# Kernel tuning notes

Measured on AMD Instinct MI355X. Metric: run time of the kernel, lower is better.

The kernel has to match this reference:

```python
import jax, jax.numpy as jnp
import numpy as np

ALPHA = 0.5      # AverageIteration limiting_alpha = max_alpha = 0.5
MAX_ITER = 50    # solver max_iter (tol-based early stop replaced by fixed count)
M = 0.1          # monotonicity margin: mu_inf(W) = 1 - m


def _make_W(A, m):
    # NEMON inf-norm parameterization: keep off-diagonal of A, set diagonal
    # W_ii = (1-m) - sum_j |offdiag_ij| so that mu_inf(W) = 1 - m exactly.
    d = jnp.diag(A)
    off = A - jnp.diag(d)
    T = jnp.sum(jnp.abs(off), axis=1)
    return off + jnp.diag((1.0 - m) - T)


def setup_inputs() -> dict:
    key = jax.random.key(0)
    k1, k2, k3, k4 = jax.random.split(key, 4)
    B, in_dim, out_dim = 16384, 784, 100
    x = jax.random.uniform(k1, (B, in_dim), dtype=jnp.float32)          # pixel-like in [0,1]
    A = jax.random.normal(k2, (out_dim, out_dim), jnp.float32) / np.sqrt(out_dim)
    U = jax.random.normal(k3, (out_dim, in_dim), jnp.float32) / np.sqrt(in_dim)
    b = jax.random.normal(k4, (out_dim,), jnp.float32) * 0.01
    eps = jnp.float32(0.1)  # input perturbation radius
    return {"x": x, "eps": eps, "A": A, "U": U, "b": b}


def reference(x, eps, A, U, b):
    W = _make_W(A, M)
    # elementwise positive/negative parts for the mixed-monotone (interval) embedding
    Wp, Wn = jnp.maximum(W, 0.0), jnp.minimum(W, 0.0)
    Up, Un = jnp.maximum(U, 0.0), jnp.minimum(U, 0.0)

    xmax, xmin = jnp.max(x), jnp.min(x)
    xh = jnp.minimum(x + eps, xmax)   # upper interval endpoint
    xl = jnp.maximum(x - eps, xmin)   # lower interval endpoint

    # injection terms Ux + b, computed once (constant across iterations)
    u  = x  @ U.T + b                              # [B, out]
    uh = xh @ Up.T + xl @ Un.T + b                 # upper-bound injection
    ul = xl @ Up.T + xh @ Un.T + b                 # lower-bound injection

    z0 = jnp.zeros_like(u)

    def step(carry, _):
        z, zh, zl = carry
        zn  = jax.nn.relu(z  @ W.T  + u)
        zhn = jax.nn.relu(zh @ Wp.T + zl @ Wn.T + uh)
        zln = jax.nn.relu(zl @ Wp.T + zh @ Wn.T + ul)
        new = ((1.0 - ALPHA) * z  + ALPHA * zn,
               (1.0 - ALPHA) * zh + ALPHA * zhn,
               (1.0 - ALPHA) * zl + ALPHA * zln)
        return new, None

    (z, zh, zl), _ = jax.lax.scan(step, (z0, z0, z0), None, length=MAX_ITER)
    return jnp.stack([z, zh, zl])  # [3, B, out]: nominal / upper / lower fixed points
```

## Files before the change

kernel.cpp:

```cpp
#include <hip/hip_runtime.h>
#include <math.h>

#define B_ROWS 16384
#define IN_DIM 784
#define OUT_DIM 100
#define NITER 50

#define TB  256
#define RPB 32
#define WKP 112

typedef float  f32x4   __attribute__((ext_vector_type(4)));
typedef float  f32x16  __attribute__((ext_vector_type(16)));
typedef short  short8  __attribute__((ext_vector_type(8)));
typedef unsigned int uint4v __attribute__((ext_vector_type(4)));

#define MFMA32 __builtin_amdgcn_mfma_f32_32x32x16_bf16

#define ZP_OFF 0
#define SH_OFF 8192
#define SL_OFF 16384
#define DH_OFF 24576
#define DL_OFF 32768
#define BUF_SZ 40960
#define LDS_TOTAL 81920

#define WPAD_F 16
#define UPAD_F (16 + 128 * WKP)

__device__ __forceinline__ unsigned enc_f(float f) {
  unsigned u = __float_as_uint(f);
  return (u & 0x80000000u) ? ~u : (u | 0x80000000u);
}
__device__ __forceinline__ float dec_f(unsigned e) {
  unsigned u = (e & 0x80000000u) ? (e ^ 0x80000000u) : ~e;
  return __uint_as_float(u);
}
__device__ __forceinline__ unsigned pk(float f1, float f0) {
  return __builtin_amdgcn_perm(__float_as_uint(f1), __float_as_uint(f0), 0x07060302u);
}
__device__ __forceinline__ short8 pack8(f32x4 a, f32x4 b) {
  uint4v u;
  u[0] = pk(a[1], a[0]); u[1] = pk(a[3], a[2]);
  u[2] = pk(b[1], b[0]); u[3] = pk(b[3], b[2]);
  return __builtin_bit_cast(short8, u);
}

__global__ void k_init(unsigned* wsu) {
  wsu[0] = 0u;
  wsu[1] = 0xFFFFFFFFu;
}

__global__ void k_minmax(const float4* __restrict__ x4, unsigned* __restrict__ wsu) {
  float mx = -3.4e38f, mn = 3.4e38f;
  const int n4 = (B_ROWS * IN_DIM) / 4;
  for (int i = blockIdx.x * blockDim.x + threadIdx.x; i < n4; i += gridDim.x * blockDim.x) {
    float4 v = x4[i];
    mx = fmaxf(mx, fmaxf(fmaxf(v.x, v.y), fmaxf(v.z, v.w)));
    mn = fminf(mn, fminf(fminf(v.x, v.y), fminf(v.z, v.w)));
  }
  #pragma unroll
  for (int o = 32; o; o >>= 1) {
    mx = fmaxf(mx, __shfl_xor(mx, o));
    mn = fminf(mn, __shfl_xor(mn, o));
  }
  __shared__ float smx[8], smn[8];
  int wid = threadIdx.x >> 6;
  if ((threadIdx.x & 63) == 0) { smx[wid] = mx; smn[wid] = mn; }
  __syncthreads();
  if (threadIdx.x == 0) {
    int nw = blockDim.x >> 6;
    for (int w = 1; w < nw; ++w) { mx = fmaxf(mx, smx[w]); mn = fminf(mn, smn[w]); }
    atomicMax(&wsu[0], enc_f(mx));
    atomicMin(&wsu[1], enc_f(mn));
  }
}

__global__ void k_wbuild(const float* __restrict__ A, float* __restrict__ Wpad) {
  int c = threadIdx.x;
  if (c < OUT_DIM) {
    float T = 0.f;
    for (int j = 0; j < OUT_DIM; ++j)
      if (j != c) T += fabsf(A[c * OUT_DIM + j]);
    for (int k = 0; k < WKP; ++k) {
      float v = 0.f;
      if (k < OUT_DIM) v = (k == c) ? (0.9f - T) : A[c * OUT_DIM + k];
      Wpad[c * WKP + k] = v;
    }
  } else if (c < 128) {
    for (int k = 0; k < WKP; ++k) Wpad[c * WKP + k] = 0.f;
  }
}

__global__ void k_upad(const float* __restrict__ U, float* __restrict__ Upad) {
  int i = blockIdx.x * blockDim.x + threadIdx.x;
  if (i < 128 * IN_DIM) {
    int n = i / IN_DIM;
    Upad[i] = (n < OUT_DIM) ? U[i] : 0.f;
  }
}

__launch_bounds__(TB, 2)
__global__ void k_main(const float* __restrict__ x, const float* __restrict__ epsp,
                       const float* __restrict__ bvec, const float* __restrict__ Wpad,
                       const unsigned* __restrict__ wsu, const float* __restrict__ Upad,
                       float* __restrict__ out) {
  extern __shared__ char lds[];
  const int t    = threadIdx.x;
  const int l    = t & 63;
  const int nt   = t >> 6;
  const int lm   = l & 31;
  const int hi   = l >> 5;
  const int r0   = blockIdx.x * RPB;
  const int mrow = lm;
  const int nbase = nt * 32;

  short8 whc[7], wlc[7];
  #pragma unroll
  for (int c = 0; c < 7; ++c) {
    const float* wp = Wpad + (nbase + lm) * WKP + c * 16 + hi * 8;
    f32x4 a = *(const f32x4*)wp;
    f32x4 b = *(const f32x4*)(wp + 4);
    whc[c] = pack8(a, b);
    f32x4 alo, blo;
    #pragma unroll
    for (int j = 0; j < 4; ++j) {
      alo[j] = a[j] - __uint_as_float(__float_as_uint(a[j]) & 0xffff0000u);
      blo[j] = b[j] - __uint_as_float(__float_as_uint(b[j]) & 0xffff0000u);
    }
    wlc[c] = pack8(alo, blo);
  }

  for (int e = t * 16; e < BUF_SZ; e += TB * 16)
    *(f32x4*)(lds + e) = (f32x4){0.f, 0.f, 0.f, 0.f};
  __syncthreads();

  const float eps  = epsp[0];
  const float xmax = dec_f(wsu[0]);
  const float xmin = dec_f(wsu[1]);

  f32x16 inj_u, inj_s, inj_d;
  #pragma unroll
  for (int r = 0; r < 16; ++r) {
    int n = nbase + (r & 3) + 8 * (r >> 2) + 4 * hi;
    float bn = (n < OUT_DIM) ? bvec[n] : 0.f;
    inj_u[r] = bn; inj_s[r] = bn; inj_d[r] = 0.f;
  }

  for (int c = 0; c < 49; ++c) {
    const int koff = c * 16 + hi * 8;
    const float* xp = x + (size_t)(r0 + mrow) * IN_DIM + koff;
    f32x4 x0 = *(const f32x4*)xp;
    f32x4 x1 = *(const f32x4*)(xp + 4);
    f32x4 xs0, xs1, xd0, xd1;
    #pragma unroll
    for (int j = 0; j < 4; ++j) {
      float h0 = fminf(x0[j] + eps, xmax), l0 = fmaxf(x0[j] - eps, xmin);
      float h1 = fminf(x1[j] + eps, xmax), l1 = fmaxf(x1[j] - eps, xmin);
      xs0[j] = 0.5f * (h0 + l0); xd0[j] = 0.5f * (h0 - l0);
      xs1[j] = 0.5f * (h1 + l1); xd1[j] = 0.5f * (h1 - l1);
    }
    short8 xa  = pack8(x0, x1);
    short8 xsa = pack8(xs0, xs1);
    short8 xda = pack8(xd0, xd1);

    const float* up = Upad + (size_t)(nbase + lm) * IN_DIM + koff;
    f32x4 u0 = *(const f32x4*)up;
    f32x4 u1 = *(const f32x4*)(up + 4);
    short8 ub = pack8(u0, u1);
    short8 au = __builtin_bit_cast(short8,
        __builtin_bit_cast(uint4v, ub) & 0x7fff7fffu);

    inj_u = MFMA32(ub, xa,  inj_u, 0, 0, 0);
    inj_s = MFMA32(ub, xsa, inj_s, 0, 0, 0);
    inj_d = MFMA32(au, xda, inj_d, 0, 0, 0);
  }

  f32x16 zc, sc, dc;
  #pragma unroll
  for (int r = 0; r < 16; ++r) { zc[r] = 0.f; sc[r] = 0.f; dc[r] = 0.f; }

  const int kr    = ((mrow & 7) << 1) | ((mrow >> 3) & 1);
  const int sbase = mrow * 256;

  #pragma unroll 1
  for (int it = 0; it < NITER; ++it) {
    const int rbase = (it & 1) ? BUF_SZ : 0;
    const int wbase = rbase ^ BUF_SZ;
    const bool last = (it == NITER - 1);

    {
      f32x16 az = inj_u;
      #pragma unroll
      for (int c = 0; c < 7; ++c) {
        const char* rp_ = lds + rbase + sbase + (((2 * c + hi) ^ kr) << 4);
        short8 z8 = *(const short8*)(rp_ + ZP_OFF);
        az = MFMA32(whc[c], z8, az, 0, 0, 0);
      }
      #pragma unroll
      for (int r = 0; r < 16; ++r)
        zc[r] = 0.5f * zc[r] + 0.5f * fmaxf(az[r], 0.f);
    }
    if (!last) {
      #pragma unroll
      for (int qd = 0; qd < 4; ++qd) {
        const int r = qd * 4;
        char* wp_ = lds + wbase + sbase + (((nt * 4 + qd) ^ kr) << 4) + hi * 8;
        *(uint2*)(wp_ + ZP_OFF) =
            make_uint2(pk(zc[r + 1], zc[r]), pk(zc[r + 3], zc[r + 2]));
      }
    }
    {
      f32x16 as4 = inj_s, ad4 = inj_d;
      #pragma unroll
      for (int c = 0; c < 7; ++c) {
        const char* rp_ = lds + rbase + sbase + (((2 * c + hi) ^ kr) << 4);
        short8 sh8 = *(const short8*)(rp_ + SH_OFF);
        short8 sl8 = *(const short8*)(rp_ + SL_OFF);
        short8 dh8 = *(const short8*)(rp_ + DH_OFF);
        short8 dl8 = *(const short8*)(rp_ + DL_OFF);
        short8 wh = whc[c], wl = wlc[c];
        uint4v whu = __builtin_bit_cast(uint4v, wh);
        short8 awh = __builtin_bit_cast(short8, whu & 0x7fff7fffu);
        short8 awl = __builtin_bit_cast(short8,
            __builtin_bit_cast(uint4v, wl) ^ (whu & 0x80008000u));
        as4 = MFMA32(wh,  sh8, as4, 0, 0, 0);
        as4 = MFMA32(wl,  sh8, as4, 0, 0, 0);
        as4 = MFMA32(wh,  sl8, as4, 0, 0, 0);
        ad4 = MFMA32(awh, dh8, ad4, 0, 0, 0);
        ad4 = MFMA32(awl, dh8, ad4, 0, 0, 0);
        ad4 = MFMA32(awh, dl8, ad4, 0, 0, 0);
      }
      #pragma unroll
      for (int r = 0; r < 16; ++r) {
        float rp = fmaxf(as4[r] + ad4[r], 0.f);
        float rm = fmaxf(as4[r] - ad4[r], 0.f);
        sc[r] = 0.5f * sc[r] + 0.25f * (rp + rm);
        dc[r] = 0.5f * dc[r] + 0.25f * (rp - rm);
      }
    }
    if (!last) {
      #pragma unroll
      for (int qd = 0; qd < 4; ++qd) {
        const int r = qd * 4;
        char* wp_ = lds + wbase + sbase + (((nt * 4 + qd) ^ kr) << 4) + hi * 8;
        f32x4 hi4, lo4;
        #pragma unroll
        for (int j = 0; j < 4; ++j) {
          hi4[j] = __uint_as_float(__float_as_uint(sc[r + j]) & 0xffff0000u);
          lo4[j] = sc[r + j] - hi4[j];
        }
        *(uint2*)(wp_ + SH_OFF) = make_uint2(pk(hi4[1], hi4[0]), pk(hi4[3], hi4[2]));
        *(uint2*)(wp_ + SL_OFF) = make_uint2(pk(lo4[1], lo4[0]), pk(lo4[3], lo4[2]));
        #pragma unroll
        for (int j = 0; j < 4; ++j) {
          hi4[j] = __uint_as_float(__float_as_uint(dc[r + j]) & 0xffff0000u);
          lo4[j] = dc[r + j] - hi4[j];
        }
        *(uint2*)(wp_ + DH_OFF) = make_uint2(pk(hi4[1], hi4[0]), pk(hi4[3], hi4[2]));
        *(uint2*)(wp_ + DL_OFF) = make_uint2(pk(lo4[1], lo4[0]), pk(lo4[3], lo4[2]));
      }
      __syncthreads();
    }
  }

  const size_t PL = (size_t)B_ROWS * OUT_DIM;
  #pragma unroll
  for (int qd = 0; qd < 4; ++qd) {
    const int nb = nbase + qd * 8 + hi * 4;
    if (nb < OUT_DIM) {
      const int r = qd * 4;
      const size_t gi = (size_t)(r0 + mrow) * OUT_DIM + nb;
      f32x4 zv, hv, lv;
      #pragma unroll
      for (int j = 0; j < 4; ++j) {
        zv[j] = zc[r + j];
        hv[j] = sc[r + j] + dc[r + j];
        lv[j] = sc[r + j] - dc[r + j];
      }
      *(f32x4*)(out + gi)          = zv;
      *(f32x4*)(out + PL + gi)     = hv;
      *(f32x4*)(out + 2 * PL + gi) = lv;
    }
  }
}

extern "C" void kernel_launch(void* const* d_in, const int* in_sizes, int n_in,
                              void* d_out, int out_size, void* d_ws, size_t ws_size,
                              hipStream_t stream) {
  const float* x   = (const float*)d_in[0];
  const float* eps = (const float*)d_in[1];
  const float* A   = (const float*)d_in[2];
  const float* U   = (const float*)d_in[3];
  const float* b   = (const float*)d_in[4];
  float* out = (float*)d_out;

  unsigned* wsu  = (unsigned*)d_ws;
  float*    Wpad = (float*)d_ws + WPAD_F;
  float*    Upad = (float*)d_ws + UPAD_F;

  (void)hipFuncSetAttribute((const void*)k_main,
                            hipFuncAttributeMaxDynamicSharedMemorySize, LDS_TOTAL);

  k_init<<<1, 1, 0, stream>>>(wsu);
  k_minmax<<<1024, 256, 0, stream>>>((const float4*)x, wsu);
  k_wbuild<<<1, 128, 0, stream>>>(A, Wpad);
  k_upad<<<(128 * IN_DIM + 255) / 256, 256, 0, stream>>>(U, Upad);
  k_main<<<B_ROWS / RPB, TB, LDS_TOTAL, stream>>>(x, eps, b, Wpad, wsu, Upad, out);
}
```

Measured before the change: 251.6 us.

## Use two waves per block, each computing two 32-column output tiles

Halves the block to 128 threads so each wave owns 64 output columns (two 32x32 MFMA tiles) and reuses each LDS-loaded z/s/d fragment for both tiles. This halves LDS reads per MFMA and the number of waves that synchronise per iteration. In exchange it doubles per-thread register use (weights, accumulators, state), relaxes launch bounds to one block per SIMD, and halves the waves available to hide MFMA and LDS latency.

After: 305.6 us. 1.21x slower.

```diff
diff --git a/kernel.cpp b/kernel.cpp
--- a/kernel.cpp
+++ b/kernel.cpp
@@ -6,7 +6,7 @@
 #define OUT_DIM 100
 #define NITER 50
 
-#define TB  256
+#define TB  128
 #define RPB 32
 #define WKP 112
 
@@ -100,7 +100,7 @@
   }
 }
 
-__launch_bounds__(TB, 2)
+__launch_bounds__(TB, 1)
 __global__ void k_main(const float* __restrict__ x, const float* __restrict__ epsp,
                        const float* __restrict__ bvec, const float* __restrict__ Wpad,
                        const unsigned* __restrict__ wsu, const float* __restrict__ Upad,
@@ -113,22 +113,24 @@
   const int hi   = l >> 5;
   const int r0   = blockIdx.x * RPB;
   const int mrow = lm;
-  const int nbase = nt * 32;
-
-  short8 whc[7], wlc[7];
-  #pragma unroll
-  for (int c = 0; c < 7; ++c) {
-    const float* wp = Wpad + (nbase + lm) * WKP + c * 16 + hi * 8;
-    f32x4 a = *(const f32x4*)wp;
-    f32x4 b = *(const f32x4*)(wp + 4);
-    whc[c] = pack8(a, b);
-    f32x4 alo, blo;
-    #pragma unroll
-    for (int j = 0; j < 4; ++j) {
-      alo[j] = a[j] - __uint_as_float(__float_as_uint(a[j]) & 0xffff0000u);
-      blo[j] = b[j] - __uint_as_float(__float_as_uint(b[j]) & 0xffff0000u);
-    }
-    wlc[c] = pack8(alo, blo);
+
+  short8 whc[2][7], wlc[2][7];
+  #pragma unroll
+  for (int q = 0; q < 2; ++q) {
+    #pragma unroll
+    for (int c = 0; c < 7; ++c) {
+      const float* wp = Wpad + (nt * 64 + q * 32 + lm) * WKP + c * 16 + hi * 8;
+      f32x4 a = *(const f32x4*)wp;
+      f32x4 b = *(const f32x4*)(wp + 4);
+      whc[q][c] = pack8(a, b);
+      f32x4 alo, blo;
+      #pragma unroll
+      for (int j = 0; j < 4; ++j) {
+        alo[j] = a[j] - __uint_as_float(__float_as_uint(a[j]) & 0xffff0000u);
+        blo[j] = b[j] - __uint_as_float(__float_as_uint(b[j]) & 0xffff0000u);
+      }
+      wlc[q][c] = pack8(alo, blo);
+    }
   }
 
   for (int e = t * 16; e < BUF_SZ; e += TB * 16)
@@ -139,12 +141,15 @@
   const float xmax = dec_f(wsu[0]);
   const float xmin = dec_f(wsu[1]);
 
-  f32x16 inj_u, inj_s, inj_d;
-  #pragma unroll
-  for (int r = 0; r < 16; ++r) {
-    int n = nbase + (r & 3) + 8 * (r >> 2) + 4 * hi;
-    float bn = (n < OUT_DIM) ? bvec[n] : 0.f;
-    inj_u[r] = bn; inj_s[r] = bn; inj_d[r] = 0.f;
+  f32x16 inj_u[2], inj_s[2], inj_d[2];
+  #pragma unroll
+  for (int q = 0; q < 2; ++q) {
+    #pragma unroll
+    for (int r = 0; r < 16; ++r) {
+      int n = nt * 64 + q * 32 + (r & 3) + 8 * (r >> 2) + 4 * hi;
+      float bn = (n < OUT_DIM) ? bvec[n] : 0.f;
+      inj_u[q][r] = bn; inj_s[q][r] = bn; inj_d[q][r] = 0.f;
+    }
   }
 
   for (int c = 0; c < 49; ++c) {
@@ -164,21 +169,26 @@
     short8 xsa = pack8(xs0, xs1);
     short8 xda = pack8(xd0, xd1);
 
-    const float* up = Upad + (size_t)(nbase + lm) * IN_DIM + koff;
-    f32x4 u0 = *(const f32x4*)up;
-    f32x4 u1 = *(const f32x4*)(up + 4);
-    short8 ub = pack8(u0, u1);
-    short8 au = __builtin_bit_cast(short8,
-        __builtin_bit_cast(uint4v, ub) & 0x7fff7fffu);
-
-    inj_u = MFMA32(ub, xa,  inj_u, 0, 0, 0);
-    inj_s = MFMA32(ub, xsa, inj_s, 0, 0, 0);
-    inj_d = MFMA32(au, xda, inj_d, 0, 0, 0);
-  }
-
-  f32x16 zc, sc, dc;
-  #pragma unroll
-  for (int r = 0; r < 16; ++r) { zc[r] = 0.f; sc[r] = 0.f; dc[r] = 0.f; }
+    #pragma unroll
+    for (int q = 0; q < 2; ++q) {
+      const float* up = Upad + (size_t)(nt * 64 + q * 32 + lm) * IN_DIM + koff;
+      f32x4 u0 = *(const f32x4*)up;
+      f32x4 u1 = *(const f32x4*)(up + 4);
+      short8 ub = pack8(u0, u1);
+      short8 au = __builtin_bit_cast(short8,
+          __builtin_bit_cast(uint4v, ub) & 0x7fff7fffu);
+      inj_u[q] = MFMA32(ub, xa,  inj_u[q], 0, 0, 0);
+      inj_s[q] = MFMA32(ub, xsa, inj_s[q], 0, 0, 0);
+      inj_d[q] = MFMA32(au, xda, inj_d[q], 0, 0, 0);
+    }
+  }
+
+  f32x16 zc[2], sc[2], dc[2];
+  #pragma unroll
+  for (int q = 0; q < 2; ++q) {
+    #pragma unroll
+    for (int r = 0; r < 16; ++r) { zc[q][r] = 0.f; sc[q][r] = 0.f; dc[q][r] = 0.f; }
+  }
 
   const int kr    = ((mrow & 7) << 1) | ((mrow >> 3) & 1);
   const int sbase = mrow * 256;
@@ -190,28 +200,35 @@
     const bool last = (it == NITER - 1);
 
     {
-      f32x16 az = inj_u;
+      f32x16 az0 = inj_u[0], az1 = inj_u[1];
       #pragma unroll
       for (int c = 0; c < 7; ++c) {
         const char* rp_ = lds + rbase + sbase + (((2 * c + hi) ^ kr) << 4);
         short8 z8 = *(const short8*)(rp_ + ZP_OFF);
-        az = MFMA32(whc[c], z8, az, 0, 0, 0);
-      }
-      #pragma unroll
-      for (int r = 0; r < 16; ++r)
-        zc[r] = 0.5f * zc[r] + 0.5f * fmaxf(az[r], 0.f);
+        az0 = MFMA32(whc[0][c], z8, az0, 0, 0, 0);
+        az1 = MFMA32(whc[1][c], z8, az1, 0, 0, 0);
+      }
+      #pragma unroll
+      for (int r = 0; r < 16; ++r) {
+        zc[0][r] = 0.5f * zc[0][r] + 0.5f * fmaxf(az0[r], 0.f);
+        zc[1][r] = 0.5f * zc[1][r] + 0.5f * fmaxf(az1[r], 0.f);
+      }
     }
     if (!last) {
       #pragma unroll
-      for (int qd = 0; qd < 4; ++qd) {
-        const int r = qd * 4;
-        char* wp_ = lds + wbase + sbase + (((nt * 4 + qd) ^ kr) << 4) + hi * 8;
-        *(uint2*)(wp_ + ZP_OFF) =
-            make_uint2(pk(zc[r + 1], zc[r]), pk(zc[r + 3], zc[r + 2]));
+      for (int q = 0; q < 2; ++q) {
+        #pragma unroll
+        for (int qd = 0; qd < 4; ++qd) {
+          const int r = qd * 4;
+          char* wp_ = lds + wbase + sbase +
+                      ((((nt * 2 + q) * 4 + qd) ^ kr) << 4) + hi * 8;
+          *(uint2*)(wp_ + ZP_OFF) =
+              make_uint2(pk(zc[q][r + 1], zc[q][r]), pk(zc[q][r + 3], zc[q][r + 2]));
+        }
       }
     }
     {
-      f32x16 as4 = inj_s, ad4 = inj_d;
+      f32x16 as0 = inj_s[0], ad0 = inj_d[0], as1 = inj_s[1], ad1 = inj_d[1];
       #pragma unroll
       for (int c = 0; c < 7; ++c) {
         const char* rp_ = lds + rbase + sbase + (((2 * c + hi) ^ kr) << 4);
@@ -219,68 +236,91 @@
         short8 sl8 = *(const short8*)(rp_ + SL_OFF);
         short8 dh8 = *(const short8*)(rp_ + DH_OFF);
         short8 dl8 = *(const short8*)(rp_ + DL_OFF);
-        short8 wh = whc[c], wl = wlc[c];
-        uint4v whu = __builtin_bit_cast(uint4v, wh);
-        short8 awh = __builtin_bit_cast(short8, whu & 0x7fff7fffu);
-        short8 awl = __builtin_bit_cast(short8,
-            __builtin_bit_cast(uint4v, wl) ^ (whu & 0x80008000u));
-        as4 = MFMA32(wh,  sh8, as4, 0, 0, 0);
-        as4 = MFMA32(wl,  sh8, as4, 0, 0, 0);
-        as4 = MFMA32(wh,  sl8, as4, 0, 0, 0);
-        ad4 = MFMA32(awh, dh8, ad4, 0, 0, 0);
-        ad4 = MFMA32(awl, dh8, ad4, 0, 0, 0);
-        ad4 = MFMA32(awh, dl8, ad4, 0, 0, 0);
+        #pragma unroll
+        for (int q = 0; q < 2; ++q) {
+          short8 wh = whc[q][c], wl = wlc[q][c];
+          uint4v whu = __builtin_bit_cast(uint4v, wh);
+          short8 awh = __builtin_bit_cast(short8, whu & 0x7fff7fffu);
+          short8 awl = __builtin_bit_cast(short8,
+              __builtin_bit_cast(uint4v, wl) ^ (whu & 0x80008000u));
+          if (q == 0) {
+            as0 = MFMA32(wh,  sh8, as0, 0, 0, 0);
+            as0 = MFMA32(wl,  sh8, as0, 0, 0, 0);
+            as0 = MFMA32(wh,  sl8, as0, 0, 0, 0);
+            ad0 = MFMA32(awh, dh8, ad0, 0, 0, 0);
+            ad0 = MFMA32(awl, dh8, ad0, 0, 0, 0);
+            ad0 = MFMA32(awh, dl8, ad0, 0, 0, 0);
+          } else {
+            as1 = MFMA32(wh,  sh8, as1, 0, 0, 0);
+            as1 = MFMA32(wl,  sh8, as1, 0, 0, 0);
+            as1 = MFMA32(wh,  sl8, as1, 0, 0, 0);
+            ad1 = MFMA32(awh, dh8, ad1, 0, 0, 0);
+            ad1 = MFMA32(awl, dh8, ad1, 0, 0, 0);
+            ad1 = MFMA32(awh, dl8, ad1, 0, 0, 0);
+          }
+        }
       }
       #pragma unroll
       for (int r = 0; r < 16; ++r) {
-        float rp = fmaxf(as4[r] + ad4[r], 0.f);
-        float rm = fmaxf(as4[r] - ad4[r], 0.f);
-        sc[r] = 0.5f * sc[r] + 0.25f * (rp + rm);
-        dc[r] = 0.5f * dc[r] + 0.25f * (rp - rm);
+        float rp0 = fmaxf(as0[r] + ad0[r], 0.f);
+        float rm0 = fmaxf(as0[r] - ad0[r], 0.f);
+        sc[0][r] = 0.5f * sc[0][r] + 0.25f * (rp0 + rm0);
+        dc[0][r] = 0.5f * dc[0][r] + 0.25f * (rp0 - rm0);
+        float rp1 = fmaxf(as1[r] + ad1[r], 0.f);
+        float rm1 = fmaxf(as1[r] - ad1[r], 0.f);
+        sc[1][r] = 0.5f * sc[1][r] + 0.25f * (rp1 + rm1);
+        dc[1][r] = 0.5f * dc[1][r] + 0.25f * (rp1 - rm1);
       }
     }
     if (!last) {
       #pragma unroll
-      for (int qd = 0; qd < 4; ++qd) {
+      for (int q = 0; q < 2; ++q) {
+        #pragma unroll
+        for (int qd = 0; qd < 4; ++qd) {
+          const int r = qd * 4;
+          char* wp_ = lds + wbase + sbase +
+                      ((((nt * 2 + q) * 4 + qd) ^ kr) << 4) + hi * 8;
+          f32x4 hi4, lo4;
+          #pragma unroll
+          for (int j = 0; j < 4; ++j) {
+            hi4[j] = __uint_as_float(__float_as_uint(sc[q][r + j]) & 0xffff0000u);
+            lo4[j] = sc[q][r + j] - hi4[j];
+          }
+          *(uint2*)(wp_ + SH_OFF) = make_uint2(pk(hi4[1], hi4[0]), pk(hi4[3], hi4[2]));
+          *(uint2*)(wp_ + SL_OFF) = make_uint2(pk(lo4[1], lo4[0]), pk(lo4[3], lo4[2]));
+          #pragma unroll
+          for (int j = 0; j < 4; ++j) {
+            hi4[j] = __uint_as_float(__float_as_uint(dc[q][r + j]) & 0xffff0000u);
+            lo4[j] = dc[q][r + j] - hi4[j];
+          }
+          *(uint2*)(wp_ + DH_OFF) = make_uint2(pk(hi4[1], hi4[0]), pk(hi4[3], hi4[2]));
+          *(uint2*)(wp_ + DL_OFF) = make_uint2(pk(lo4[1], lo4[0]), pk(lo4[3], lo4[2]));
+        }
+      }
+      __syncthreads();
+    }
+  }
+
+  const size_t PL = (size_t)B_ROWS * OUT_DIM;
+  #pragma unroll
+  for (int q = 0; q < 2; ++q) {
+    #pragma unroll
+    for (int qd = 0; qd < 4; ++qd) {
+      const int nb = nt * 64 + q * 32 + qd * 8 + hi * 4;
+      if (nb < OUT_DIM) {
         const int r = qd * 4;
-        char* wp_ = lds + wbase + sbase + (((nt * 4 + qd) ^ kr) << 4) + hi * 8;
-        f32x4 hi4, lo4;
+        const size_t gi = (size_t)(r0 + mrow) * OUT_DIM + nb;
+        f32x4 zv, hv, lv;
         #pragma unroll
         for (int j = 0; j < 4; ++j) {
-          hi4[j] = __uint_as_float(__float_as_uint(sc[r + j]) & 0xffff0000u);
-          lo4[j] = sc[r + j] - hi4[j];
+          zv[j] = zc[q][r + j];
+          hv[j] = sc[q][r + j] + dc[q][r + j];
+          lv[j] = sc[q][r + j] - dc[q][r + j];
         }
-        *(uint2*)(wp_ + SH_OFF) = make_uint2(pk(hi4[1], hi4[0]), pk(hi4[3], hi4[2]));
-        *(uint2*)(wp_ + SL_OFF) = make_uint2(pk(lo4[1], lo4[0]), pk(lo4[3], lo4[2]));
-        #pragma unroll
-        for (int j = 0; j < 4; ++j) {
-          hi4[j] = __uint_as_float(__float_as_uint(dc[r + j]) & 0xffff0000u);
-          lo4[j] = dc[r + j] - hi4[j];
-        }
-        *(uint2*)(wp_ + DH_OFF) = make_uint2(pk(hi4[1], hi4[0]), pk(hi4[3], hi4[2]));
-        *(uint2*)(wp_ + DL_OFF) = make_uint2(pk(lo4[1], lo4[0]), pk(lo4[3], lo4[2]));
-      }
-      __syncthreads();
-    }
-  }
-
-  const size_t PL = (size_t)B_ROWS * OUT_DIM;
-  #pragma unroll
-  for (int qd = 0; qd < 4; ++qd) {
-    const int nb = nbase + qd * 8 + hi * 4;
-    if (nb < OUT_DIM) {
-      const int r = qd * 4;
-      const size_t gi = (size_t)(r0 + mrow) * OUT_DIM + nb;
-      f32x4 zv, hv, lv;
-      #pragma unroll
-      for (int j = 0; j < 4; ++j) {
-        zv[j] = zc[r + j];
-        hv[j] = sc[r + j] + dc[r + j];
-        lv[j] = sc[r + j] - dc[r + j];
-      }
-      *(f32x4*)(out + gi)          = zv;
-      *(f32x4*)(out + PL + gi)     = hv;
-      *(f32x4*)(out + 2 * PL + gi) = lv;
+        *(f32x4*)(out + gi)          = zv;
+        *(f32x4*)(out + PL + gi)     = hv;
+        *(f32x4*)(out + 2 * PL + gi) = lv;
+      }
     }
   }
 }
```
